# Kernel tuning notes

Hardware: AMD Instinct MI355X
Metric: run time of the kernel (lower is better)

Reference implementation:

```python
import jax, jax.numpy as jnp
import numpy as np

B, S, E, H = 2, 2048, 2048, 32
D = E // H  # head_dim = 64
SCALE = D ** -0.5


def setup_inputs() -> dict:
    key = jax.random.key(0)
    ks = jax.random.split(key, 9)
    std = E ** -0.5
    return {
        "hidden_states": jax.random.normal(ks[0], (B, S, E), dtype=jnp.float32),
        "Wq": jax.random.normal(ks[1], (E, E), dtype=jnp.float32) * std,
        "bq": jax.random.normal(ks[2], (E,), dtype=jnp.float32) * 0.02,
        "Wk": jax.random.normal(ks[3], (E, E), dtype=jnp.float32) * std,
        "bk": jax.random.normal(ks[4], (E,), dtype=jnp.float32) * 0.02,
        "Wv": jax.random.normal(ks[5], (E, E), dtype=jnp.float32) * std,
        "bv": jax.random.normal(ks[6], (E,), dtype=jnp.float32) * 0.02,
        "Wo": jax.random.normal(ks[7], (E, E), dtype=jnp.float32) * std,
        "bo": jax.random.normal(ks[8], (E,), dtype=jnp.float32) * 0.02,
    }


def reference(hidden_states, Wq, bq, Wk, bk, Wv, bv, Wo, bo):
    # QKV projections (torch Linear: x @ W.T + b)
    q = hidden_states @ Wq.T + bq  # [B,S,E]
    k = hidden_states @ Wk.T + bk
    v = hidden_states @ Wv.T + bv
    # split heads -> [B,S,H,D]
    q = q.reshape(B, S, H, D)
    k = k.reshape(B, S, H, D)
    v = v.reshape(B, S, H, D)
    # causal scaled dot-product attention (prefill path of paged attention)
    scores = jnp.einsum("bqhd,bkhd->bhqk", q, k) * SCALE  # [B,H,S,S]
    causal = jnp.tril(jnp.ones((S, S), dtype=bool))
    scores = jnp.where(causal, scores, jnp.finfo(scores.dtype).min)
    probs = jax.nn.softmax(scores, axis=-1)
    attn = jnp.einsum("bhqk,bkhd->bqhd", probs, v).reshape(B, S, E)
    # output projection
    return attn @ Wo.T + bo
```

## Files before the change

kernel.cpp:

```cpp
#include <hip/hip_runtime.h>
#include <hip/hip_bf16.h>

#define B_ 2
#define S_ 2048
#define E_ 2048
#define H_ 32
#define D_ 64
#define SCALE_L2E 0.18033688f

typedef __attribute__((ext_vector_type(8))) short short8_t;
typedef __attribute__((ext_vector_type(4))) float float4_t;
typedef __attribute__((ext_vector_type(16))) float f32x16;
typedef unsigned int uint;
typedef __attribute__((ext_vector_type(4))) uint uint4_t;

__device__ __forceinline__ short f2bf(float f) {
  union { float f; unsigned u; } x; x.f = f;
  unsigned r = x.u + 0x7fffu + ((x.u >> 16) & 1u);
  return (short)(r >> 16);
}

__device__ __forceinline__ void gload_lds16(const void* g, void* l) {
  __builtin_amdgcn_global_load_lds((const __attribute__((address_space(1))) void*)g,
                                   (__attribute__((address_space(3))) void*)l, 16, 0, 0);
}

__device__ __forceinline__ uint cvt_pk_bf16(float lo, float hi) {
  uint r;
  asm volatile("v_cvt_pk_bf16_f32 %0, %1, %2" : "=v"(r) : "v"(lo), "v"(hi));
  return r;
}

__device__ __forceinline__ void pl32swap(uint& a, uint& b) {
  asm volatile("v_permlane32_swap_b32 %0, %1" : "+v"(a), "+v"(b));
}

__device__ __forceinline__ f32x16 zero16() {
  f32x16 v;
#pragma unroll
  for (int i = 0; i < 16; ++i) v[i] = 0.f;
  return v;
}

__global__ void cast_bf16_kernel(const float* __restrict__ in, short* __restrict__ out, int n4) {
  const int stride = gridDim.x * blockDim.x;
  for (int j = blockIdx.x * blockDim.x + threadIdx.x; j < n4; j += stride) {
    const float4 v = ((const float4*)in)[j];
    short4 r;
    r.x = f2bf(v.x); r.y = f2bf(v.y); r.z = f2bf(v.z); r.w = f2bf(v.w);
    ((short4*)out)[j] = r;
  }
}

__global__ void cast3_bf16(const float* __restrict__ a, const float* __restrict__ b,
                           const float* __restrict__ c, short* __restrict__ out) {
  constexpr int n4 = (E_ * E_) / 4;
  const int stride = gridDim.x * blockDim.x;
  for (int j = blockIdx.x * blockDim.x + threadIdx.x; j < 3 * n4; j += stride) {
    const float* src = (j < n4) ? a : (j < 2 * n4 ? b : c);
    const int idx = j & (n4 - 1);
    const float4 v = ((const float4*)src)[idx];
    short4 r;
    r.x = f2bf(v.x); r.y = f2bf(v.y); r.z = f2bf(v.z); r.w = f2bf(v.w);
    ((short4*)out)[j] = r;
  }
}

template <int MODE>
__global__ __launch_bounds__(512, 2) void gemm8(const short* __restrict__ A,
                                                const short* __restrict__ Wt,
                                                const float* __restrict__ bq,
                                                const float* __restrict__ bk,
                                                const float* __restrict__ bv,
                                                short* __restrict__ Qb,
                                                short* __restrict__ Kb,
                                                short* __restrict__ Vb,
                                                float* __restrict__ Fout) {
  extern __shared__ __align__(16) char lds[];
  constexpr int K = E_, NT = K / 64;
  const int tid = threadIdx.x, w = tid >> 6, lane = tid & 63;
  const int wr = w >> 2, wc = w & 3;
  const int m0 = blockIdx.y * 128, n0 = blockIdx.x * 256;
  const int l15 = lane & 15, l4 = lane >> 4;

  const int sr = lane >> 2;
  const int ss = lane & 3;
  const char* aBase;
  const char* bBase0;
  const char* bBase1;
  {
    const int ra = w * 16 + sr;
    aBase = (const char*)A + (size_t)(m0 + ra) * (K * 2) + ((ss ^ ((ra >> 1) & 3)) * 16);
    const int rb0 = 0 * 128 + w * 16 + sr;
    bBase0 = (const char*)Wt + (size_t)(n0 + rb0) * (K * 2) + ((ss ^ ((rb0 >> 1) & 3)) * 16);
    const int rb1 = 1 * 128 + w * 16 + sr;
    bBase1 = (const char*)Wt + (size_t)(n0 + rb1) * (K * 2) + ((ss ^ ((rb1 >> 1) & 3)) * 16);
  }

  auto stageA = [&](int dbuf, int ks, int kt) {
    gload_lds16(aBase + kt * 128 + ks * 64, lds + (dbuf * 2 + ks) * 8192 + w * 1024);
  };
  auto stageB = [&](int dbuf, int ks, int kt) {
    char* base = lds + 32768 + (dbuf * 2 + ks) * 16384 + w * 1024;
    gload_lds16(bBase0 + kt * 128 + ks * 64, base);
    gload_lds16(bBase1 + kt * 128 + ks * 64, base + 8192);
  };
  auto ldA = [&](int dbuf, int ks, int i) {
    const int lr = wr * 64 + i * 16 + l15;
    return *(const short8_t*)(lds + (dbuf * 2 + ks) * 8192 + lr * 64 +
                              ((l4 * 16) ^ (((lr >> 1) & 3) << 4)));
  };
  auto ldB = [&](int dbuf, int ks, int j) {
    const int lc = wc * 64 + j * 16 + l15;
    return *(const short8_t*)(lds + 32768 + (dbuf * 2 + ks) * 16384 + lc * 64 +
                              ((l4 * 16) ^ (((lc >> 1) & 3) << 4)));
  };

  float4_t acc[4][4];
#pragma unroll
  for (int i = 0; i < 4; ++i)
#pragma unroll
    for (int j = 0; j < 4; ++j) acc[i][j] = (float4_t){0.f, 0.f, 0.f, 0.f};

  stageA(0, 0, 0);
  stageB(0, 0, 0);
  stageA(0, 1, 0);
  stageB(0, 1, 0);

  short8_t a_[4], b_[4];
  for (int t = 0; t < NT; ++t) {
    const int c = t & 1;
#pragma unroll
    for (int ks = 0; ks < 2; ++ks) {
      if (t + 1 < NT) {
        stageA(c ^ 1, ks, t + 1);
        stageB(c ^ 1, ks, t + 1);
        asm volatile("s_waitcnt vmcnt(6)" ::: "memory");
      } else if (ks == 0) {
        asm volatile("s_waitcnt vmcnt(3)" ::: "memory");
      } else {
        asm volatile("s_waitcnt vmcnt(0)" ::: "memory");
      }
      __builtin_amdgcn_s_barrier();
      asm volatile("" ::: "memory");
#pragma unroll
      for (int i = 0; i < 4; ++i) a_[i] = ldA(c, ks, i);
#pragma unroll
      for (int j = 0; j < 4; ++j) b_[j] = ldB(c, ks, j);
      asm volatile("s_waitcnt lgkmcnt(0)" ::: "memory");
      __builtin_amdgcn_sched_barrier(0);
      __builtin_amdgcn_s_setprio(1);
#pragma unroll
      for (int i = 0; i < 4; ++i)
#pragma unroll
        for (int j = 0; j < 4; ++j)
          acc[i][j] = __builtin_amdgcn_mfma_f32_16x16x32_bf16(a_[i], b_[j], acc[i][j], 0, 0, 0);
      __builtin_amdgcn_s_setprio(0);
    }
  }

  const int rg = l4 * 4;
  if (MODE == 1) {
#pragma unroll
    for (int j = 0; j < 4; ++j) {
      const int col = n0 + wc * 64 + j * 16 + l15;
      const float bvv = bq[col];
#pragma unroll
      for (int i = 0; i < 4; ++i)
#pragma unroll
        for (int ii = 0; ii < 4; ++ii)
          Fout[(size_t)(m0 + wr * 64 + i * 16 + rg + ii) * E_ + col] = acc[i][j][ii] + bvv;
    }
  } else {
    const int seg = n0 >> 11;
    const int ncol = n0 & 2047;
    if (seg == 2) {
      __syncthreads();
      char* qt = lds + w * 8192;
      const int b = m0 >> 11;
      const int mloc = m0 & (S_ - 1);
#pragma unroll
      for (int j = 0; j < 4; ++j) {
        const float bvv = bv[ncol + wc * 64 + j * 16 + l15];
        const int nl = j * 16 + l15;
#pragma unroll
        for (int i = 0; i < 4; ++i) {
          short4 v;
          v.x = f2bf(acc[i][j][0] + bvv);
          v.y = f2bf(acc[i][j][1] + bvv);
          v.z = f2bf(acc[i][j][2] + bvv);
          v.w = f2bf(acc[i][j][3] + bvv);
          *(short4*)(qt + nl * 128 + (((i * 16 + rg) * 2) ^ ((nl & 7) << 4))) = v;
        }
      }
      asm volatile("s_waitcnt lgkmcnt(0)" ::: "memory");
      __builtin_amdgcn_sched_barrier(0);
#pragma unroll
      for (int p = 0; p < 8; ++p) {
        const int rowd = p * 8 + (lane >> 3);
        const short8_t vv =
            *(const short8_t*)(qt + rowd * 128 + (((lane & 7) * 16) ^ ((rowd & 7) << 4)));
        *(short8_t*)(Vb + ((size_t)(b * E_ + ncol + wc * 64 + rowd)) * S_ + mloc + wr * 64 +
                     (lane & 7) * 8) = vv;
      }
    } else {
      const float* bias = seg ? bk : bq;
      short* Out = seg ? Kb : Qb;
      const float sc = seg ? 1.0f : SCALE_L2E;
#pragma unroll
      for (int j = 0; j < 4; ++j) {
        const int col = ncol + wc * 64 + j * 16 + l15;
        const float bvv = bias[col];
#pragma unroll
        for (int i = 0; i < 4; ++i)
#pragma unroll
          for (int ii = 0; ii < 4; ++ii)
            Out[(size_t)(m0 + wr * 64 + i * 16 + rg + ii) * E_ + col] =
                f2bf((acc[i][j][ii] + bvv) * sc);
      }
    }
  }
}

__global__ __launch_bounds__(512, 2) void attn_fwd(const short* __restrict__ Qg,
                                                   const short* __restrict__ Kg,
                                                   const short* __restrict__ Vt,
                                                   short* __restrict__ Og) {
  __shared__ __align__(16) short lds[16384];
  const int tid = threadIdx.x, w = tid >> 6, lane = tid & 63;
  const int l31 = lane & 31, hh = lane >> 5;
  const int bh = blockIdx.x;
  const int b = bh >> 5, h = bh & 31;
  const int pq = blockIdx.y;

  const char* Kgb = (const char*)(Kg + (size_t)b * S_ * E_ + h * D_);
  const char* Vgb = (const char*)(Vt + (size_t)bh * 64 * S_);

  const int srow = w * 8 + (lane >> 3);
  const int sb = (lane & 7) * 16;
  const int ssw = (srow & 7) << 4;

#pragma unroll 1
  for (int ph = 0; ph < 2; ++ph) {
    const int qt = ph ? (7 - pq) : pq;
    const int q0 = qt * 256;
    const int qwmin = q0 + w * 32;
    const int qg = qwmin + l31;

    const short* qr = Qg + ((size_t)(b * S_ + qg)) * E_ + h * D_;
    short8_t qf[4];
#pragma unroll
    for (int dblk = 0; dblk < 4; ++dblk)
      qf[dblk] = *(const short8_t*)(qr + dblk * 16 + hh * 8);

    f32x16 o0 = zero16(), o1 = zero16();
    float m_run = -1e30f, l_run = 0.f;

    const int nt = 4 * qt + 4;
    const int ntw = (qwmin + 31) / 64 + 1;

    gload_lds16(Kgb + (size_t)srow * 4096 + (sb ^ ssw), lds + w * 512);
    gload_lds16(Vgb + (size_t)srow * 4096 + (sb ^ ssw), lds + 4096 + w * 512);
    __syncthreads();

    int cur = 0;
    for (int t = 0; t < nt; ++t) {
      if (t + 1 < nt) {
        const int k0n = (t + 1) * 64;
        short* kb = lds + (cur ^ 1) * 8192 + w * 512;
        gload_lds16(Kgb + (size_t)(k0n + srow) * 4096 + (sb ^ ssw), kb);
        gload_lds16(Vgb + (size_t)srow * 4096 + (size_t)k0n * 2 + (sb ^ ssw), kb + 4096);
      }

      if (t < ntw) {
        const int k0 = t * 64;
        const char* Kc = (const char*)lds + cur * 16384;
        const char* Vc = Kc + 8192;
        const int xs = (l31 & 7) << 4;

        f32x16 st0 = zero16(), st1 = zero16();
#pragma unroll
        for (int dblk = 0; dblk < 4; ++dblk) {
          const int off = (dblk * 32 + hh * 16) ^ xs;
          const short8_t kf0 = *(const short8_t*)(Kc + l31 * 128 + off);
          const short8_t kf1 = *(const short8_t*)(Kc + (32 + l31) * 128 + off);
          st0 = __builtin_amdgcn_mfma_f32_32x32x16_bf16(kf0, qf[dblk], st0, 0, 0, 0);
          st1 = __builtin_amdgcn_mfma_f32_32x32x16_bf16(kf1, qf[dblk], st1, 0, 0, 0);
        }

        if (k0 + 63 > qwmin) {
#pragma unroll
          for (int r = 0; r < 16; ++r) {
            const int kvr = k0 + ((r & 3) + 8 * (r >> 2) + 4 * hh);
            if (kvr > qg) st0[r] = -1e30f;
            if (kvr + 32 > qg) st1[r] = -1e30f;
          }
        }

        float mv = -1e30f;
#pragma unroll
        for (int r = 0; r < 16; ++r) mv = fmaxf(mv, fmaxf(st0[r], st1[r]));
        mv = fmaxf(mv, __shfl_xor(mv, 32));
        const float mnew = fmaxf(m_run, mv);
        const float alpha = exp2f(m_run - mnew);
        m_run = mnew;
        float sum = 0.f;
#pragma unroll
        for (int r = 0; r < 16; ++r) {
          st0[r] = exp2f(st0[r] - mnew);
          st1[r] = exp2f(st1[r] - mnew);
          sum += st0[r] + st1[r];
        }
        sum += __shfl_xor(sum, 32);
        l_run = l_run * alpha + sum;
        o0 = o0 * alpha;
        o1 = o1 * alpha;

        uint pk_[16];
#pragma unroll
        for (int j = 0; j < 8; ++j) pk_[j] = cvt_pk_bf16(st0[2 * j], st0[2 * j + 1]);
#pragma unroll
        for (int j = 0; j < 8; ++j) pk_[8 + j] = cvt_pk_bf16(st1[2 * j], st1[2 * j + 1]);
        pl32swap(pk_[0], pk_[2]);  pl32swap(pk_[1], pk_[3]);
        pl32swap(pk_[4], pk_[6]);  pl32swap(pk_[5], pk_[7]);
        pl32swap(pk_[8], pk_[10]); pl32swap(pk_[9], pk_[11]);
        pl32swap(pk_[12], pk_[14]); pl32swap(pk_[13], pk_[15]);
        uint4_t paw[4];
#pragma unroll
        for (int f = 0; f < 4; ++f)
          paw[f] = (uint4_t){pk_[4 * f], pk_[4 * f + 1], pk_[4 * f + 2], pk_[4 * f + 3]};

#pragma unroll
        for (int kb = 0; kb < 4; ++kb) {
          const short8_t pa = *(const short8_t*)&paw[kb];
          const int off = (kb * 32 + hh * 16) ^ xs;
          const short8_t vf0 = *(const short8_t*)(Vc + l31 * 128 + off);
          const short8_t vf1 = *(const short8_t*)(Vc + (32 + l31) * 128 + off);
          o0 = __builtin_amdgcn_mfma_f32_32x32x16_bf16(vf0, pa, o0, 0, 0, 0);
          o1 = __builtin_amdgcn_mfma_f32_32x32x16_bf16(vf1, pa, o1, 0, 0, 0);
        }
      }

      __syncthreads();
      cur ^= 1;
    }

    {
      short* ow = lds + w * 2048;
      const float inv = 1.0f / l_run;
#pragma unroll
      for (int r = 0; r < 16; ++r) {
        const int d = (r & 3) + 8 * (r >> 2) + 4 * hh;
        const int x = (l31 & 7) << 4;
        *(short*)((char*)ow + l31 * 128 + ((d * 2) ^ x)) = f2bf(o0[r] * inv);
        *(short*)((char*)ow + l31 * 128 + (((d + 32) * 2) ^ x)) = f2bf(o1[r] * inv);
      }
#pragma unroll
      for (int pz = 0; pz < 4; ++pz) {
        const int qloc = pz * 8 + (lane >> 3);
        const int sbyte = (lane & 7) * 16;
        const short8_t vv = *(const short8_t*)((char*)ow + qloc * 128 + (sbyte ^ ((qloc & 7) << 4)));
        *(short8_t*)(Og + ((size_t)(b * S_ + q0 + w * 32 + qloc)) * E_ + h * 64 + (lane & 7) * 8) = vv;
      }
    }
    __syncthreads();
  }
}

extern "C" void kernel_launch(void* const* d_in, const int* in_sizes, int n_in,
                              void* d_out, int out_size, void* d_ws, size_t ws_size,
                              hipStream_t stream) {
  const float* X  = (const float*)d_in[0];
  const float* Wq = (const float*)d_in[1];
  const float* bq = (const float*)d_in[2];
  const float* Wk = (const float*)d_in[3];
  const float* bk = (const float*)d_in[4];
  const float* Wv = (const float*)d_in[5];
  const float* bv = (const float*)d_in[6];
  const float* Wo = (const float*)d_in[7];
  const float* bo = (const float*)d_in[8];

  const size_t NX = (size_t)B_ * S_ * E_;
  const size_t NW = (size_t)E_ * E_;

  short* ws = (short*)d_ws;
  short* Xb = ws;
  short* Wb = Xb + NX;
  short* Kb = Wb + 3 * NW;
  short* Vb = Kb + NX;
  short* Qb = (short*)d_out;
  short* Ab = Xb;

  (void)hipFuncSetAttribute((const void*)gemm8<0>,
                            hipFuncAttributeMaxDynamicSharedMemorySize, 98304);
  (void)hipFuncSetAttribute((const void*)gemm8<1>,
                            hipFuncAttributeMaxDynamicSharedMemorySize, 98304);

  cast_bf16_kernel<<<2048, 256, 0, stream>>>(X, Xb, (int)(NX / 4));
  cast3_bf16<<<3072, 256, 0, stream>>>(Wq, Wk, Wv, Wb);

  gemm8<0><<<dim3(3 * E_ / 256, B_ * S_ / 128), 512, 98304, stream>>>(Xb, Wb, bq, bk, bv,
                                                                      Qb, Kb, Vb, nullptr);

  cast_bf16_kernel<<<1024, 256, 0, stream>>>(Wo, Wb, (int)(NW / 4));

  attn_fwd<<<dim3(B_ * H_, 4), 512, 0, stream>>>(Qb, Kb, Vb, Ab);

  gemm8<1><<<dim3(E_ / 256, B_ * S_ / 128), 512, 98304, stream>>>(Ab, Wb, bo, nullptr, nullptr,
                                                                  nullptr, nullptr, nullptr,
                                                                  (float*)d_out);
}
```

Before: 254.9 us.

## Widen fused QKV GEMM tile to 128x384 with per-column-block epilogue

Replaces the templated 128x256 GEMM used for the fused QKV projection with a dedicated kernel that uses 128x384 tiles. Each wave now holds a 4x6 grid of MFMA accumulators, and each block stages three B sub-tiles. The grid shrinks from 768 to 512 blocks, which is meant to improve wave quantization across the CUs and increase reuse of each A tile. The epilogue now picks Q, K or V per 16-column group and does the V transpose through a small per-wave scratch area. The trade-off is 128 KB of LDS per block and higher register pressure, which may limit occupancy.

```diff
diff --git a/kernel.cpp b/kernel.cpp
--- a/kernel.cpp
+++ b/kernel.cpp
@@ -66,16 +66,152 @@
   }
 }
 
-template <int MODE>
-__global__ __launch_bounds__(512, 2) void gemm8(const short* __restrict__ A,
-                                                const short* __restrict__ Wt,
-                                                const float* __restrict__ bq,
-                                                const float* __restrict__ bk,
-                                                const float* __restrict__ bv,
-                                                short* __restrict__ Qb,
-                                                short* __restrict__ Kb,
-                                                short* __restrict__ Vb,
-                                                float* __restrict__ Fout) {
+__global__ __launch_bounds__(512, 2) void gemm384_qkv(const short* __restrict__ A,
+                                                      const short* __restrict__ Wt,
+                                                      const float* __restrict__ bq,
+                                                      const float* __restrict__ bk,
+                                                      const float* __restrict__ bv,
+                                                      short* __restrict__ Qb,
+                                                      short* __restrict__ Kb,
+                                                      short* __restrict__ Vb) {
+  extern __shared__ __align__(16) char lds[];
+  constexpr int K = E_, NT = K / 64;
+  const int tid = threadIdx.x, w = tid >> 6, lane = tid & 63;
+  const int wr = w >> 2, wc = w & 3;
+  const int m0 = blockIdx.y * 128, n0 = blockIdx.x * 384;
+  const int l15 = lane & 15, l4 = lane >> 4;
+
+  const int sr = lane >> 2;
+  const int ss = lane & 3;
+  const char* aBase;
+  const char* bBase[3];
+  {
+    const int ra = w * 16 + sr;
+    aBase = (const char*)A + (size_t)(m0 + ra) * (K * 2) + ((ss ^ ((ra >> 1) & 3)) * 16);
+#pragma unroll
+    for (int g = 0; g < 3; ++g) {
+      const int rb = g * 128 + w * 16 + sr;
+      bBase[g] = (const char*)Wt + (size_t)(n0 + rb) * (K * 2) + ((ss ^ ((rb >> 1) & 3)) * 16);
+    }
+  }
+
+  auto stageA = [&](int buf, int ks, int kt) {
+    gload_lds16(aBase + kt * 128 + ks * 64, lds + (buf * 2 + ks) * 8192 + w * 1024);
+  };
+  auto stageB = [&](int buf, int ks, int kt) {
+    char* base = lds + 32768 + (buf * 2 + ks) * 24576 + w * 1024;
+#pragma unroll
+    for (int g = 0; g < 3; ++g)
+      gload_lds16(bBase[g] + kt * 128 + ks * 64, base + g * 8192);
+  };
+  auto ldA = [&](int buf, int ks, int i) {
+    const int lr = wr * 64 + i * 16 + l15;
+    return *(const short8_t*)(lds + (buf * 2 + ks) * 8192 + lr * 64 +
+                              ((l4 * 16) ^ (((lr >> 1) & 3) << 4)));
+  };
+  auto ldB = [&](int buf, int ks, int j) {
+    const int lc = wc * 96 + j * 16 + l15;
+    return *(const short8_t*)(lds + 32768 + (buf * 2 + ks) * 24576 + lc * 64 +
+                              ((l4 * 16) ^ (((lc >> 1) & 3) << 4)));
+  };
+
+  float4_t acc[4][6];
+#pragma unroll
+  for (int i = 0; i < 4; ++i)
+#pragma unroll
+    for (int j = 0; j < 6; ++j) acc[i][j] = (float4_t){0.f, 0.f, 0.f, 0.f};
+
+  stageA(0, 0, 0);
+  stageB(0, 0, 0);
+  stageA(0, 1, 0);
+  stageB(0, 1, 0);
+
+  short8_t a_[4], b_[6];
+  for (int t = 0; t < NT; ++t) {
+    const int c = t & 1;
+#pragma unroll
+    for (int ks = 0; ks < 2; ++ks) {
+      if (t + 1 < NT) {
+        stageA(c ^ 1, ks, t + 1);
+        stageB(c ^ 1, ks, t + 1);
+        asm volatile("s_waitcnt vmcnt(8)" ::: "memory");
+      } else if (ks == 0) {
+        asm volatile("s_waitcnt vmcnt(4)" ::: "memory");
+      } else {
+        asm volatile("s_waitcnt vmcnt(0)" ::: "memory");
+      }
+      __builtin_amdgcn_s_barrier();
+      asm volatile("" ::: "memory");
+#pragma unroll
+      for (int i = 0; i < 4; ++i) a_[i] = ldA(c, ks, i);
+#pragma unroll
+      for (int j = 0; j < 6; ++j) b_[j] = ldB(c, ks, j);
+      asm volatile("s_waitcnt lgkmcnt(0)" ::: "memory");
+      __builtin_amdgcn_sched_barrier(0);
+      __builtin_amdgcn_s_setprio(1);
+#pragma unroll
+      for (int i = 0; i < 4; ++i)
+#pragma unroll
+        for (int j = 0; j < 6; ++j)
+          acc[i][j] = __builtin_amdgcn_mfma_f32_16x16x32_bf16(a_[i], b_[j], acc[i][j], 0, 0, 0);
+      __builtin_amdgcn_s_setprio(0);
+    }
+  }
+
+  __syncthreads();
+  const int rg = l4 * 4;
+  const int b = m0 >> 11;
+  const int mloc = m0 & (S_ - 1);
+  char* scratch = lds + w * 2048;
+#pragma unroll
+  for (int j = 0; j < 6; ++j) {
+    const int gc0 = n0 + wc * 96 + j * 16;
+    const int seg = gc0 >> 11;
+    const int ncol = gc0 & 2047;
+    if (seg == 2) {
+      const float bvv = bv[ncol + l15];
+      asm volatile("" ::: "memory");
+#pragma unroll
+      for (int i = 0; i < 4; ++i) {
+        short4 v;
+        v.x = f2bf(acc[i][j][0] + bvv);
+        v.y = f2bf(acc[i][j][1] + bvv);
+        v.z = f2bf(acc[i][j][2] + bvv);
+        v.w = f2bf(acc[i][j][3] + bvv);
+        *(short4*)(scratch + l15 * 128 + (((i * 16 + rg) * 2) ^ ((l15 & 7) << 4))) = v;
+      }
+      asm volatile("s_waitcnt lgkmcnt(0)" ::: "memory");
+      __builtin_amdgcn_sched_barrier(0);
+#pragma unroll
+      for (int half = 0; half < 2; ++half) {
+        const int n = (lane >> 3) + half * 8;
+        const int mb = (lane & 7) * 16;
+        const short8_t vv =
+            *(const short8_t*)(scratch + n * 128 + (mb ^ ((n & 7) << 4)));
+        *(short8_t*)(Vb + ((size_t)(b * E_ + ncol + n)) * S_ + mloc + wr * 64 + (mb >> 1)) = vv;
+      }
+      asm volatile("s_waitcnt lgkmcnt(0)" ::: "memory");
+      __builtin_amdgcn_sched_barrier(0);
+    } else {
+      const float* bias = seg ? bk : bq;
+      short* Out = seg ? Kb : Qb;
+      const float sc = seg ? 1.0f : SCALE_L2E;
+      const int col = ncol + l15;
+      const float bvv = bias[col];
+#pragma unroll
+      for (int i = 0; i < 4; ++i)
+#pragma unroll
+        for (int ii = 0; ii < 4; ++ii)
+          Out[(size_t)(m0 + wr * 64 + i * 16 + rg + ii) * E_ + col] =
+              f2bf((acc[i][j][ii] + bvv) * sc);
+    }
+  }
+}
+
+__global__ __launch_bounds__(512, 2) void gemm_o8(const short* __restrict__ A,
+                                                  const short* __restrict__ Wt,
+                                                  const float* __restrict__ bias,
+                                                  float* __restrict__ Fout) {
   extern __shared__ __align__(16) char lds[];
   constexpr int K = E_, NT = K / 64;
   const int tid = threadIdx.x, w = tid >> 6, lane = tid & 63;
@@ -91,9 +227,9 @@
   {
     const int ra = w * 16 + sr;
     aBase = (const char*)A + (size_t)(m0 + ra) * (K * 2) + ((ss ^ ((ra >> 1) & 3)) * 16);
-    const int rb0 = 0 * 128 + w * 16 + sr;
+    const int rb0 = w * 16 + sr;
     bBase0 = (const char*)Wt + (size_t)(n0 + rb0) * (K * 2) + ((ss ^ ((rb0 >> 1) & 3)) * 16);
-    const int rb1 = 1 * 128 + w * 16 + sr;
+    const int rb1 = 128 + w * 16 + sr;
     bBase1 = (const char*)Wt + (size_t)(n0 + rb1) * (K * 2) + ((ss ^ ((rb1 >> 1) & 3)) * 16);
   }
 
@@ -160,65 +296,15 @@
   }
 
   const int rg = l4 * 4;
-  if (MODE == 1) {
-#pragma unroll
-    for (int j = 0; j < 4; ++j) {
-      const int col = n0 + wc * 64 + j * 16 + l15;
-      const float bvv = bq[col];
-#pragma unroll
-      for (int i = 0; i < 4; ++i)
-#pragma unroll
-        for (int ii = 0; ii < 4; ++ii)
-          Fout[(size_t)(m0 + wr * 64 + i * 16 + rg + ii) * E_ + col] = acc[i][j][ii] + bvv;
-    }
-  } else {
-    const int seg = n0 >> 11;
-    const int ncol = n0 & 2047;
-    if (seg == 2) {
-      __syncthreads();
-      char* qt = lds + w * 8192;
-      const int b = m0 >> 11;
-      const int mloc = m0 & (S_ - 1);
-#pragma unroll
-      for (int j = 0; j < 4; ++j) {
-        const float bvv = bv[ncol + wc * 64 + j * 16 + l15];
-        const int nl = j * 16 + l15;
-#pragma unroll
-        for (int i = 0; i < 4; ++i) {
-          short4 v;
-          v.x = f2bf(acc[i][j][0] + bvv);
-          v.y = f2bf(acc[i][j][1] + bvv);
-          v.z = f2bf(acc[i][j][2] + bvv);
-          v.w = f2bf(acc[i][j][3] + bvv);
-          *(short4*)(qt + nl * 128 + (((i * 16 + rg) * 2) ^ ((nl & 7) << 4))) = v;
-        }
-      }
-      asm volatile("s_waitcnt lgkmcnt(0)" ::: "memory");
-      __builtin_amdgcn_sched_barrier(0);
-#pragma unroll
-      for (int p = 0; p < 8; ++p) {
-        const int rowd = p * 8 + (lane >> 3);
-        const short8_t vv =
-            *(const short8_t*)(qt + rowd * 128 + (((lane & 7) * 16) ^ ((rowd & 7) << 4)));
-        *(short8_t*)(Vb + ((size_t)(b * E_ + ncol + wc * 64 + rowd)) * S_ + mloc + wr * 64 +
-                     (lane & 7) * 8) = vv;
-      }
-    } else {
-      const float* bias = seg ? bk : bq;
-      short* Out = seg ? Kb : Qb;
-      const float sc = seg ? 1.0f : SCALE_L2E;
-#pragma unroll
-      for (int j = 0; j < 4; ++j) {
-        const int col = ncol + wc * 64 + j * 16 + l15;
-        const float bvv = bias[col];
-#pragma unroll
-        for (int i = 0; i < 4; ++i)
-#pragma unroll
-          for (int ii = 0; ii < 4; ++ii)
-            Out[(size_t)(m0 + wr * 64 + i * 16 + rg + ii) * E_ + col] =
-                f2bf((acc[i][j][ii] + bvv) * sc);
-      }
-    }
+#pragma unroll
+  for (int j = 0; j < 4; ++j) {
+    const int col = n0 + wc * 64 + j * 16 + l15;
+    const float bvv = bias[col];
+#pragma unroll
+    for (int i = 0; i < 4; ++i)
+#pragma unroll
+      for (int ii = 0; ii < 4; ++ii)
+        Fout[(size_t)(m0 + wr * 64 + i * 16 + rg + ii) * E_ + col] = acc[i][j][ii] + bvv;
   }
 }
 
@@ -391,22 +477,19 @@
   short* Qb = (short*)d_out;
   short* Ab = Xb;
 
-  (void)hipFuncSetAttribute((const void*)gemm8<0>,
-                            hipFuncAttributeMaxDynamicSharedMemorySize, 98304);
-  (void)hipFuncSetAttribute((const void*)gemm8<1>,
+  (void)hipFuncSetAttribute((const void*)gemm384_qkv,
+                            hipFuncAttributeMaxDynamicSharedMemorySize, 131072);
+  (void)hipFuncSetAttribute((const void*)gemm_o8,
                             hipFuncAttributeMaxDynamicSharedMemorySize, 98304);
 
   cast_bf16_kernel<<<2048, 256, 0, stream>>>(X, Xb, (int)(NX / 4));
   cast3_bf16<<<3072, 256, 0, stream>>>(Wq, Wk, Wv, Wb);
 
-  gemm8<0><<<dim3(3 * E_ / 256, B_ * S_ / 128), 512, 98304, stream>>>(Xb, Wb, bq, bk, bv,
-                                                                      Qb, Kb, Vb, nullptr);
+  gemm384_qkv<<<dim3(16, 32), 512, 131072, stream>>>(Xb, Wb, bq, bk, bv, Qb, Kb, Vb);
 
   cast_bf16_kernel<<<1024, 256, 0, stream>>>(Wo, Wb, (int)(NW / 4));
 
   attn_fwd<<<dim3(B_ * H_, 4), 512, 0, stream>>>(Qb, Kb, Vb, Ab);
 
-  gemm8<1><<<dim3(E_ / 256, B_ * S_ / 128), 512, 98304, stream>>>(Ab, Wb, bo, nullptr, nullptr,
-                                                                  nullptr, nullptr, nullptr,
-                                                                  (float*)d_out);
-}
+  gemm_o8<<<dim3(E_ / 256, B_ * S_ / 128), 512, 98304, stream>>>(Ab, Wb, bo, (float*)d_out);
+}
```

Measured after the change: 251.2 us. No clear change (-1.4%).
